# Kernel optimization log

Hardware: AMD Instinct MI355X
Metric: run time of the kernel (lower is better)

Reference implementation:

```python
import jax, jax.numpy as jnp
import numpy as np

B, S, D = 4, 2048, 1024
H, DK, DV = 16, 64, 64
LN_EPS = 1e-5


def setup_inputs() -> dict:
    key = jax.random.key(0)
    ks = jax.random.split(key, 6)
    x = jax.random.normal(ks[0], (B, S, D), dtype=jnp.float32)
    # causal mask: True = masked position (j > i), broadcast over batch
    causal = jnp.triu(jnp.ones((S, S), dtype=bool), k=1)
    attention_mask = jnp.broadcast_to(causal, (B, S, S))
    scale = 1.0 / np.sqrt(D)
    w_q = jax.random.normal(ks[1], (D, H * DK), dtype=jnp.float32) * scale
    w_k = jax.random.normal(ks[2], (D, H * DK), dtype=jnp.float32) * scale
    w_v = jax.random.normal(ks[3], (D, H * DV), dtype=jnp.float32) * scale
    w_fc = jax.random.normal(ks[4], (H * DV, D), dtype=jnp.float32) * (1.0 / np.sqrt(H * DV))
    ln_gamma = jnp.ones((D,), dtype=jnp.float32)
    ln_beta = jnp.zeros((D,), dtype=jnp.float32)
    return {"x": x, "attention_mask": attention_mask, "w_q": w_q, "w_k": w_k,
            "w_v": w_v, "w_fc": w_fc, "ln_gamma": ln_gamma, "ln_beta": ln_beta}


def _layernorm(y, gamma, beta):
    mu = jnp.mean(y, axis=-1, keepdims=True)
    var = jnp.mean(jnp.square(y - mu), axis=-1, keepdims=True)
    return (y - mu) * jax.lax.rsqrt(var + LN_EPS) * gamma + beta


def reference(x, attention_mask, w_q, w_k, w_v, w_fc, ln_gamma, ln_beta):
    b, s, _ = x.shape
    # projections -> [b, h, s, dk/dv]
    q = (x @ w_q).reshape(b, s, H, DK).transpose(0, 2, 1, 3)
    k = (x @ w_k).reshape(b, s, H, DK).transpose(0, 2, 1, 3)
    v = (x @ w_v).reshape(b, s, H, DV).transpose(0, 2, 1, 3)
    # scaled dot-product attention with mask (True -> -1e9)
    scores = jnp.einsum('bhqd,bhkd->bhqk', q, k) / np.sqrt(DK)
    scores = jnp.where(attention_mask[:, None, :, :], jnp.float32(-1e9), scores)
    attn = jax.nn.softmax(scores, axis=-1)
    context = jnp.einsum('bhqk,bhkd->bhqd', attn, v)
    context = context.transpose(0, 2, 1, 3).reshape(b, s, H * DV)
    output = context @ w_fc
    out = _layernorm(output + x, ln_gamma, ln_beta)
    return out, attn
```

## Files before the change

### kernel.cpp

```cpp
#include <hip/hip_runtime.h>
#include <stdint.h>

#define S_LEN 2048
#define NHEAD 16

typedef short short8 __attribute__((ext_vector_type(8)));
typedef float f32x4 __attribute__((ext_vector_type(4)));
typedef unsigned short u16;

typedef __attribute__((address_space(1))) uint32_t AS1u32;
typedef __attribute__((address_space(3))) uint32_t AS3u32;

#define MFMA16(a, b, c) __builtin_amdgcn_mfma_f32_16x16x32_bf16((a), (b), (c), 0, 0, 0)

__device__ __forceinline__ void gload16(const void* g, void* l) {
  __builtin_amdgcn_global_load_lds((AS1u32*)g, (AS3u32*)l, 16, 0, 0);
}

__device__ __forceinline__ u16 f2bf(float f) {
  union { float f; uint32_t u; } c; c.f = f;
  return (u16)((c.u + 0x7fffu + ((c.u >> 16) & 1u)) >> 16);
}

__global__ __launch_bounds__(256) void prep_kernel(
    const float* __restrict__ x, u16* __restrict__ xb,
    const float* __restrict__ w0, const float* __restrict__ w1,
    const float* __restrict__ w2, const float* __restrict__ w3,
    u16* __restrict__ qkvT, u16* __restrict__ fcT) {
  __shared__ float t[32][33];
  int bid = blockIdx.x;
  if (bid < 8192) {
    size_t i = ((size_t)bid * 256 + threadIdx.x) * 4;
    f32x4 v = *(const f32x4*)(x + i);
    union { u16 h[4]; uint2 d; } o;
    o.h[0] = f2bf(v[0]); o.h[1] = f2bf(v[1]); o.h[2] = f2bf(v[2]); o.h[3] = f2bf(v[3]);
    *(uint2*)(xb + i) = o.d;
    return;
  }
  int r = bid - 8192;
  int z = r >> 10; r &= 1023;
  int bx = r & 31, by = r >> 5;
  const float* w = (z == 0) ? w0 : (z == 1) ? w1 : (z == 2) ? w2 : w3;
  u16* o = (z == 3) ? fcT : qkvT + (size_t)z * 1048576;
  float scale = (z == 0) ? 0.125f : 1.0f;
  int n0 = bx * 32, k0 = by * 32;
  int tx = threadIdx.x & 31, ty = threadIdx.x >> 5;
#pragma unroll
  for (int i = 0; i < 4; ++i) {
    int k = ty * 4 + i;
    t[k][tx] = w[(size_t)(k0 + k) * 1024 + n0 + tx];
  }
  __syncthreads();
#pragma unroll
  for (int i = 0; i < 4; ++i) {
    int n = ty * 4 + i;
    o[(size_t)(n0 + n) * 1024 + k0 + tx] = f2bf(t[tx][n] * scale);
  }
}

__device__ __forceinline__ void gemm_stage(const char* Ab, const char* Bb, u16* As, u16* Bs,
                                           int m0, int n0, int kbyte, int tid) {
#pragma unroll
  for (int i = 0; i < 2; ++i) {
    int cid = i * 256 + tid;
    int row = cid >> 2, c = cid & 3;
    int off = kbyte + ((c ^ ((row >> 1) & 3)) << 4);
    gload16(Ab + (size_t)(m0 + row) * 2048 + off, (char*)As + i * 4096 + (tid & ~63) * 16);
    gload16(Bb + (size_t)(n0 + row) * 2048 + off, (char*)Bs + i * 4096 + (tid & ~63) * 16);
  }
}

__global__ __launch_bounds__(256) void gemm_bt_kernel(
    const u16* __restrict__ A, const u16* __restrict__ BT,
    void* __restrict__ out, void* __restrict__ outv, int mode) {
  __shared__ u16 sh[128 * 128];
  u16* As = sh;
  u16* Bs = sh + 4096;
  const int tid = threadIdx.x;
  const int lane = tid & 63, wv = tid >> 6;
  const int l15 = lane & 15, h16 = lane >> 4;
  const int wr = wv >> 1, wc = wv & 1;
  const int m0 = blockIdx.x * 128, n0 = blockIdx.y * 128;
  const char* Ab = (const char*)A;
  const char* Bb = (const char*)BT;

  f32x4 acc[4][4];
#pragma unroll
  for (int i = 0; i < 4; ++i)
#pragma unroll
    for (int j = 0; j < 4; ++j) acc[i][j] = (f32x4){0.f, 0.f, 0.f, 0.f};

  gemm_stage(Ab, Bb, As, Bs, m0, n0, 0, tid);
  for (int kt = 0; kt < 32; ++kt) {
    __syncthreads();
    short8 a[4], b[4];
#pragma unroll
    for (int mf = 0; mf < 4; ++mf) {
      int row = wr * 64 + mf * 16 + l15;
      a[mf] = *(const short8*)((const char*)As + row * 64 + ((h16 ^ ((row >> 1) & 3)) << 4));
    }
#pragma unroll
    for (int nf = 0; nf < 4; ++nf) {
      int row = wc * 64 + nf * 16 + l15;
      b[nf] = *(const short8*)((const char*)Bs + row * 64 + ((h16 ^ ((row >> 1) & 3)) << 4));
    }
#pragma unroll
    for (int mf = 0; mf < 4; ++mf)
#pragma unroll
      for (int nf = 0; nf < 4; ++nf)
        acc[mf][nf] = MFMA16(a[mf], b[nf], acc[mf][nf]);
    __syncthreads();
    if (kt + 1 < 32) gemm_stage(Ab, Bb, As, Bs, m0, n0, (kt + 1) * 64, tid);
  }

  if (mode == 0 && n0 < 2048) {
    u16* o = (u16*)out;
#pragma unroll
    for (int mf = 0; mf < 4; ++mf)
#pragma unroll
      for (int nf = 0; nf < 4; ++nf)
#pragma unroll
        for (int r = 0; r < 4; ++r) {
          int row = wr * 64 + mf * 16 + 4 * h16 + r;
          int col = wc * 64 + nf * 16 + l15;
          *(u16*)((char*)sh + row * 256 + (((col >> 3) ^ (row & 7)) << 4) + (col & 7) * 2) =
              f2bf(acc[mf][nf][r]);
        }
    __syncthreads();
    int row = tid >> 1, hf = tid & 1;
    int m = m0 + row;
    int bb = m >> 11, s = m & 2047;
    int n_base = n0 + hf * 64;
    int z = n_base >> 10, nn = n_base & 1023, hh = nn >> 6;
    u16* dst = o + (size_t)z * 8388608 + (((size_t)(bb * NHEAD + hh) * S_LEN + s) << 6);
#pragma unroll
    for (int i = 0; i < 8; ++i) {
      int ch = hf * 8 + i;
      short8 v = *(const short8*)((const char*)sh + row * 256 + ((ch ^ (row & 7)) << 4));
      *(short8*)(dst + i * 8) = v;
    }
  } else if (mode == 0) {
    u16* o = (u16*)outv;
#pragma unroll
    for (int mf = 0; mf < 4; ++mf)
#pragma unroll
      for (int nf = 0; nf < 4; ++nf)
#pragma unroll
        for (int r = 0; r < 4; ++r) {
          int row = wr * 64 + mf * 16 + 4 * h16 + r;
          int col = wc * 64 + nf * 16 + l15;
          *(u16*)((char*)sh + col * 256 + (((row >> 3) ^ (col & 7)) << 4) + (row & 7) * 2) =
              f2bf(acc[mf][nf][r]);
        }
    __syncthreads();
    int col = tid >> 1, half = tid & 1;
    int bb = m0 >> 11, s0 = (m0 & 2047) + half * 64;
    int nn = n0 - 2048 + col;
    int hh = nn >> 6, dv = nn & 63;
    u16* dst = o + ((size_t)(bb * NHEAD + hh) * 64 + dv) * S_LEN + s0;
    const char* base = (const char*)sh + col * 256;
#pragma unroll
    for (int i = 0; i < 8; ++i) {
      int ch = (half * 8 + i) ^ (col & 7);
      *(short8*)(dst + i * 8) = *(const short8*)(base + (ch << 4));
    }
  } else {
    float* o = (float*)out;
#pragma unroll
    for (int mf = 0; mf < 4; ++mf)
#pragma unroll
      for (int nf = 0; nf < 4; ++nf)
#pragma unroll
        for (int r = 0; r < 4; ++r) {
          int m = m0 + wr * 64 + mf * 16 + 4 * h16 + r;
          int n = n0 + wc * 64 + nf * 16 + l15;
          o[(size_t)m * 1024 + n] = acc[mf][nf][r];
        }
  }
}

__device__ __forceinline__ void stage_qk(const char* base, int row0, u16* dst, int tid) {
#pragma unroll
  for (int i = 0; i < 2; ++i) {
    int cid = i * 512 + tid;
    int row = cid >> 3, c = cid & 7;
    gload16(base + (size_t)(row0 + row) * 128 + ((c ^ (row & 7)) << 4),
            (char*)dst + i * 8192 + (tid & ~63) * 16);
  }
}
__device__ __forceinline__ void stage_v(const char* Vb, int kv0, u16* dst, int tid) {
#pragma unroll
  for (int i = 0; i < 2; ++i) {
    int cid = i * 512 + tid;
    int row = cid >> 4, c = cid & 15;
    gload16(Vb + (size_t)row * 4096 + (size_t)kv0 * 2 + ((c ^ (row & 7)) << 4),
            (char*)dst + i * 8192 + (tid & ~63) * 16);
  }
}

__device__ __forceinline__ void qk_tile(const char* Kc, const short8* qf,
                                        f32x4* sc, int l15, int h16) {
#pragma unroll
  for (int nf = 0; nf < 8; ++nf) sc[nf] = (f32x4){0.f, 0.f, 0.f, 0.f};
#pragma unroll
  for (int ks = 0; ks < 2; ++ks)
#pragma unroll
    for (int nf = 0; nf < 8; ++nf) {
      int row = nf * 16 + l15;
      short8 kb = *(const short8*)(Kc + row * 128 + (((ks * 4 + h16) ^ (row & 7)) << 4));
      sc[nf] = MFMA16(qf[ks], kb, sc[nf]);
    }
}

__device__ __forceinline__ void attn_one(
    const u16* __restrict__ Q, const u16* __restrict__ K, const u16* __restrict__ VT,
    float* __restrict__ attn, u16* __restrict__ ctx, int qt, int bh, int tid,
    u16 (*Ks)[128 * 64], u16* Vs, u16* Ps) {
  const int lane = tid & 63, wv = tid >> 6;
  const int l15 = lane & 15, h16 = lane >> 4;
  const int w16 = wv * 16;
  const int q0 = qt * 128;
  const char* Qb = (const char*)(Q + (size_t)bh * S_LEN * 64);
  const char* Kb = (const char*)(K + (size_t)bh * S_LEN * 64);
  const char* Vb = (const char*)(VT + (size_t)bh * 64 * S_LEN);
  float* attb = attn + (size_t)bh * S_LEN * S_LEN;

  stage_qk(Qb, q0, Ps, tid);
  stage_qk(Kb, q0, Ks[0], tid);
  __syncthreads();
  short8 qf[2];
  {
    int row = w16 + l15;
    qf[0] = *(const short8*)((const char*)Ps + row * 128 + ((h16 ^ (row & 7)) << 4));
    qf[1] = *(const short8*)((const char*)Ps + row * 128 + (((4 + h16) ^ (row & 7)) << 4));
  }
  __syncthreads();

  float lsum[4] = {0.f, 0.f, 0.f, 0.f};
  int cur = 0;
  for (int t = qt; t >= 0; --t) {
    if (t > 0) stage_qk(Kb, (t - 1) * 128, Ks[cur ^ 1], tid);
    f32x4 sc[8];
    qk_tile((const char*)Ks[cur], qf, sc, l15, h16);
    if (t == qt) {
#pragma unroll
      for (int nf = 0; nf < 8; ++nf)
#pragma unroll
        for (int r = 0; r < 4; ++r)
          if (nf * 16 + l15 > w16 + 4 * h16 + r) sc[nf][r] = -1e30f;
    }
#pragma unroll
    for (int nf = 0; nf < 8; ++nf)
#pragma unroll
      for (int r = 0; r < 4; ++r) lsum[r] += __expf(sc[nf][r]);
    __syncthreads();
    cur ^= 1;
  }
  cur ^= 1;
  f32x4 ri;
#pragma unroll
  for (int r = 0; r < 4; ++r) {
    float v = lsum[r];
    v += __shfl_xor(v, 1);
    v += __shfl_xor(v, 2);
    v += __shfl_xor(v, 4);
    v += __shfl_xor(v, 8);
    ri[r] = 1.0f / v;
  }

  f32x4 cacc[4];
#pragma unroll
  for (int nf = 0; nf < 4; ++nf) cacc[nf] = (f32x4){0.f, 0.f, 0.f, 0.f};

  for (int t = 0; t <= qt; ++t) {
    const int kv0 = t * 128;
    stage_v(Vb, kv0, Vs, tid);
    f32x4 sc[8];
    qk_tile((const char*)Ks[cur], qf, sc, l15, h16);
    if (t == qt) {
#pragma unroll
      for (int nf = 0; nf < 8; ++nf)
#pragma unroll
        for (int r = 0; r < 4; ++r)
          if (nf * 16 + l15 > w16 + 4 * h16 + r) sc[nf][r] = -1e30f;
    }
    {
      float* arow = attb + (size_t)(q0 + w16 + 4 * h16) * S_LEN + kv0 + l15;
#pragma unroll
      for (int nf = 0; nf < 8; ++nf)
#pragma unroll
        for (int r = 0; r < 4; ++r) {
          float p = __expf(sc[nf][r]) * ri[r];
          int rowL = w16 + 4 * h16 + r;
          int chunk = 2 * nf + (l15 >> 3);
          *(u16*)((char*)Ps + rowL * 256 + ((chunk ^ (rowL & 7)) << 4) + (l15 & 7) * 2) = f2bf(p);
          arow[(size_t)r * S_LEN + nf * 16] = p;
        }
    }
    __syncthreads();
    if (t < qt) stage_qk(Kb, kv0 + 128, Ks[cur ^ 1], tid);
#pragma unroll
    for (int ks = 0; ks < 4; ++ks) {
      int rowP = w16 + l15;
      short8 pa = *(const short8*)((const char*)Ps + rowP * 256 + (((ks * 4 + h16) ^ (rowP & 7)) << 4));
#pragma unroll
      for (int nf = 0; nf < 4; ++nf) {
        int rowV = nf * 16 + l15;
        short8 vbf = *(const short8*)((const char*)Vs + rowV * 256 + (((ks * 4 + h16) ^ (rowV & 7)) << 4));
        cacc[nf] = MFMA16(pa, vbf, cacc[nf]);
      }
    }
    __syncthreads();
    cur ^= 1;
  }

  for (int kvt = qt + 1; kvt < 16; ++kvt) {
    const int kv0 = kvt * 128;
    int row = tid >> 2, sub = tid & 3;
    float* arow = attb + (size_t)(q0 + row) * S_LEN + kv0;
    f32x4 z = {0.f, 0.f, 0.f, 0.f};
#pragma unroll
    for (int c8 = 0; c8 < 4; ++c8) {
      int chunk = sub + 4 * c8;
      *(f32x4*)(arow + chunk * 8) = z;
      *(f32x4*)(arow + chunk * 8 + 4) = z;
    }
  }

  {
    int b = bh >> 4, hh = bh & 15;
#pragma unroll
    for (int nf = 0; nf < 4; ++nf)
#pragma unroll
      for (int r = 0; r < 4; ++r) {
        int qrow = q0 + w16 + 4 * h16 + r;
        ctx[((size_t)b * S_LEN + qrow) * 1024 + hh * 64 + nf * 16 + l15] = f2bf(cacc[nf][r]);
      }
  }
}

__global__ __launch_bounds__(512) void attn2_kernel(
    const u16* __restrict__ Q, const u16* __restrict__ K, const u16* __restrict__ VT,
    float* __restrict__ attn, u16* __restrict__ ctx) {
  __shared__ u16 Ks[2][128 * 64];
  __shared__ u16 Vs[64 * 128];
  __shared__ u16 Ps[128 * 128];
  const int tid = threadIdx.x;
  const int w = blockIdx.x;
  const int bx = (w >> 3) & 7;
  const int bh = (w & 7) + ((w >> 6) << 3);
  attn_one(Q, K, VT, attn, ctx, 15 - bx, bh, tid, Ks, Vs, Ps);
  attn_one(Q, K, VT, attn, ctx, bx, bh, tid, Ks, Vs, Ps);
}

__global__ __launch_bounds__(256) void ln_kernel(float* __restrict__ io,
                                                 const float* __restrict__ x,
                                                 const float* __restrict__ gamma,
                                                 const float* __restrict__ beta) {
  int row = blockIdx.x, tid = threadIdx.x;
  size_t base = (size_t)row * 1024 + tid * 4;
  f32x4 p = *(const f32x4*)(io + base);
  f32x4 xv = *(const f32x4*)(x + base);
  f32x4 y;
  float s1 = 0.f, s2 = 0.f;
#pragma unroll
  for (int j = 0; j < 4; ++j) {
    y[j] = p[j] + xv[j];
    s1 += y[j];
    s2 += y[j] * y[j];
  }
#pragma unroll
  for (int off = 1; off <= 32; off <<= 1) {
    s1 += __shfl_xor(s1, off);
    s2 += __shfl_xor(s2, off);
  }
  __shared__ float r1[4], r2[4];
  int w = tid >> 6;
  if ((tid & 63) == 0) { r1[w] = s1; r2[w] = s2; }
  __syncthreads();
  float S1 = r1[0] + r1[1] + r1[2] + r1[3];
  float S2 = r2[0] + r2[1] + r2[2] + r2[3];
  float mu = S1 * (1.f / 1024.f);
  float var = S2 * (1.f / 1024.f) - mu * mu;
  float rs = rsqrtf(var + 1e-5f);
  f32x4 g = *(const f32x4*)(gamma + tid * 4);
  f32x4 bt = *(const f32x4*)(beta + tid * 4);
  f32x4 o;
#pragma unroll
  for (int j = 0; j < 4; ++j) o[j] = (y[j] - mu) * rs * g[j] + bt[j];
  *(f32x4*)(io + base) = o;
}

extern "C" void kernel_launch(void* const* d_in, const int* in_sizes, int n_in,
                              void* d_out, int out_size, void* d_ws, size_t ws_size,
                              hipStream_t stream) {
  (void)in_sizes; (void)n_in; (void)out_size; (void)ws_size;
  const float* x = (const float*)d_in[0];
  const float* wq = (const float*)d_in[2];
  const float* wk = (const float*)d_in[3];
  const float* wv = (const float*)d_in[4];
  const float* wfc = (const float*)d_in[5];
  const float* gamma = (const float*)d_in[6];
  const float* beta = (const float*)d_in[7];

  char* ws = (char*)d_ws;
  u16* xb = (u16*)ws;
  u16* wqkvT = (u16*)(ws + (16u << 20));
  u16* wfcT = (u16*)(ws + (22u << 20));
  u16* qkb = (u16*)(ws + (24u << 20));
  u16* qb = qkb;
  u16* kb = qkb + (size_t)8388608;
  u16* vT = (u16*)(ws + (56u << 20));
  u16* ctx = xb;

  float* outp = (float*)d_out;
  float* attnp = outp + (size_t)4 * 2048 * 1024;

  prep_kernel<<<12288, 256, 0, stream>>>(x, xb, wq, wk, wv, wfc, wqkvT, wfcT);
  gemm_bt_kernel<<<dim3(64, 24), 256, 0, stream>>>(xb, wqkvT, qkb, vT, 0);
  attn2_kernel<<<512, 512, 0, stream>>>(qb, kb, vT, attnp, ctx);
  gemm_bt_kernel<<<dim3(64, 8), 256, 0, stream>>>(ctx, wfcT, outp, nullptr, 1);
  ln_kernel<<<8192, 256, 0, stream>>>(outp, x, gamma, beta);
}
```

Measured before the change: 473.1 us.

## Fuse row-sum passes of paired query tiles to share K tile loads

The attention kernel handles two query tiles per block (a high and a low causal tile). It previously ran a separate softmax-denominator pass for each, and now runs a single K sweep that computes row sums for both tiles from the same K fragments held in LDS. This removes the duplicated K staging and LDS reads of the low tile's first pass. It also adds a launch_bounds occupancy hint, at the cost of more live registers for the second set of Q fragments and accumulators.

```diff
diff --git a/kernel.cpp b/kernel.cpp
--- a/kernel.cpp
+++ b/kernel.cpp
@@ -212,61 +212,14 @@
     }
 }
 
-__device__ __forceinline__ void attn_one(
-    const u16* __restrict__ Q, const u16* __restrict__ K, const u16* __restrict__ VT,
-    float* __restrict__ attn, u16* __restrict__ ctx, int qt, int bh, int tid,
-    u16 (*Ks)[128 * 64], u16* Vs, u16* Ps) {
+__device__ __forceinline__ void attn_emit(
+    const char* Kb, const char* Vb, float* attb, u16* __restrict__ ctx,
+    int qt, int bh, int tid, const short8* qf, f32x4 ri,
+    u16 (*Ks)[128 * 64], u16* Vs, u16* Ps, int cur) {
   const int lane = tid & 63, wv = tid >> 6;
   const int l15 = lane & 15, h16 = lane >> 4;
   const int w16 = wv * 16;
   const int q0 = qt * 128;
-  const char* Qb = (const char*)(Q + (size_t)bh * S_LEN * 64);
-  const char* Kb = (const char*)(K + (size_t)bh * S_LEN * 64);
-  const char* Vb = (const char*)(VT + (size_t)bh * 64 * S_LEN);
-  float* attb = attn + (size_t)bh * S_LEN * S_LEN;
-
-  stage_qk(Qb, q0, Ps, tid);
-  stage_qk(Kb, q0, Ks[0], tid);
-  __syncthreads();
-  short8 qf[2];
-  {
-    int row = w16 + l15;
-    qf[0] = *(const short8*)((const char*)Ps + row * 128 + ((h16 ^ (row & 7)) << 4));
-    qf[1] = *(const short8*)((const char*)Ps + row * 128 + (((4 + h16) ^ (row & 7)) << 4));
-  }
-  __syncthreads();
-
-  float lsum[4] = {0.f, 0.f, 0.f, 0.f};
-  int cur = 0;
-  for (int t = qt; t >= 0; --t) {
-    if (t > 0) stage_qk(Kb, (t - 1) * 128, Ks[cur ^ 1], tid);
-    f32x4 sc[8];
-    qk_tile((const char*)Ks[cur], qf, sc, l15, h16);
-    if (t == qt) {
-#pragma unroll
-      for (int nf = 0; nf < 8; ++nf)
-#pragma unroll
-        for (int r = 0; r < 4; ++r)
-          if (nf * 16 + l15 > w16 + 4 * h16 + r) sc[nf][r] = -1e30f;
-    }
-#pragma unroll
-    for (int nf = 0; nf < 8; ++nf)
-#pragma unroll
-      for (int r = 0; r < 4; ++r) lsum[r] += __expf(sc[nf][r]);
-    __syncthreads();
-    cur ^= 1;
-  }
-  cur ^= 1;
-  f32x4 ri;
-#pragma unroll
-  for (int r = 0; r < 4; ++r) {
-    float v = lsum[r];
-    v += __shfl_xor(v, 1);
-    v += __shfl_xor(v, 2);
-    v += __shfl_xor(v, 4);
-    v += __shfl_xor(v, 8);
-    ri[r] = 1.0f / v;
-  }
 
   f32x4 cacc[4];
 #pragma unroll
@@ -339,7 +292,103 @@
   }
 }
 
-__global__ __launch_bounds__(512) void attn2_kernel(
+__device__ __forceinline__ void attn_pair(
+    const u16* __restrict__ Q, const u16* __restrict__ K, const u16* __restrict__ VT,
+    float* __restrict__ attn, u16* __restrict__ ctx, int qtH, int qtL, int bh, int tid,
+    u16 (*Ks)[128 * 64], u16* Vs, u16* Ps) {
+  const int lane = tid & 63, wv = tid >> 6;
+  const int l15 = lane & 15, h16 = lane >> 4;
+  const int w16 = wv * 16;
+  const char* Qb = (const char*)(Q + (size_t)bh * S_LEN * 64);
+  const char* Kb = (const char*)(K + (size_t)bh * S_LEN * 64);
+  const char* Vb = (const char*)(VT + (size_t)bh * 64 * S_LEN);
+  float* attb = attn + (size_t)bh * S_LEN * S_LEN;
+
+  stage_qk(Qb, qtH * 128, Ps, tid);
+  stage_qk(Kb, qtH * 128, Ks[0], tid);
+  __syncthreads();
+  short8 qfh[2];
+  {
+    int row = w16 + l15;
+    qfh[0] = *(const short8*)((const char*)Ps + row * 128 + ((h16 ^ (row & 7)) << 4));
+    qfh[1] = *(const short8*)((const char*)Ps + row * 128 + (((4 + h16) ^ (row & 7)) << 4));
+  }
+  __syncthreads();
+  stage_qk(Qb, qtL * 128, Ps, tid);
+  __syncthreads();
+  short8 qfl[2];
+  {
+    int row = w16 + l15;
+    qfl[0] = *(const short8*)((const char*)Ps + row * 128 + ((h16 ^ (row & 7)) << 4));
+    qfl[1] = *(const short8*)((const char*)Ps + row * 128 + (((4 + h16) ^ (row & 7)) << 4));
+  }
+  __syncthreads();
+
+  float lsH[4] = {0.f, 0.f, 0.f, 0.f};
+  float lsL[4] = {0.f, 0.f, 0.f, 0.f};
+  int cur = 0;
+  for (int t = qtH; t >= 0; --t) {
+    if (t > 0) stage_qk(Kb, (t - 1) * 128, Ks[cur ^ 1], tid);
+    const char* Kc = (const char*)Ks[cur];
+    const bool doL = (t <= qtL);
+#pragma unroll
+    for (int nf = 0; nf < 8; ++nf) {
+      int row = nf * 16 + l15;
+      short8 k0 = *(const short8*)(Kc + row * 128 + ((h16 ^ (row & 7)) << 4));
+      short8 k1 = *(const short8*)(Kc + row * 128 + (((4 + h16) ^ (row & 7)) << 4));
+      f32x4 s = {0.f, 0.f, 0.f, 0.f};
+      s = MFMA16(qfh[0], k0, s);
+      s = MFMA16(qfh[1], k1, s);
+      if (t == qtH) {
+#pragma unroll
+        for (int r = 0; r < 4; ++r)
+          if (nf * 16 + l15 > w16 + 4 * h16 + r) s[r] = -1e30f;
+      }
+#pragma unroll
+      for (int r = 0; r < 4; ++r) lsH[r] += __expf(s[r]);
+      if (doL) {
+        f32x4 sl = {0.f, 0.f, 0.f, 0.f};
+        sl = MFMA16(qfl[0], k0, sl);
+        sl = MFMA16(qfl[1], k1, sl);
+        if (t == qtL) {
+#pragma unroll
+          for (int r = 0; r < 4; ++r)
+            if (nf * 16 + l15 > w16 + 4 * h16 + r) sl[r] = -1e30f;
+        }
+#pragma unroll
+        for (int r = 0; r < 4; ++r) lsL[r] += __expf(sl[r]);
+      }
+    }
+    __syncthreads();
+    cur ^= 1;
+  }
+  cur ^= 1;
+
+  f32x4 riH, riL;
+#pragma unroll
+  for (int r = 0; r < 4; ++r) {
+    float v = lsH[r];
+    v += __shfl_xor(v, 1);
+    v += __shfl_xor(v, 2);
+    v += __shfl_xor(v, 4);
+    v += __shfl_xor(v, 8);
+    riH[r] = 1.0f / v;
+    float u = lsL[r];
+    u += __shfl_xor(u, 1);
+    u += __shfl_xor(u, 2);
+    u += __shfl_xor(u, 4);
+    u += __shfl_xor(u, 8);
+    riL[r] = 1.0f / u;
+  }
+
+  attn_emit(Kb, Vb, attb, ctx, qtH, bh, tid, qfh, riH, Ks, Vs, Ps, cur);
+
+  stage_qk(Kb, 0, Ks[0], tid);
+  __syncthreads();
+  attn_emit(Kb, Vb, attb, ctx, qtL, bh, tid, qfl, riL, Ks, Vs, Ps, 0);
+}
+
+__global__ __launch_bounds__(512, 4) void attn2_kernel(
     const u16* __restrict__ Q, const u16* __restrict__ K, const u16* __restrict__ VT,
     float* __restrict__ attn, u16* __restrict__ ctx) {
   __shared__ u16 Ks[2][128 * 64];
@@ -349,8 +398,7 @@
   const int w = blockIdx.x;
   const int bx = (w >> 3) & 7;
   const int bh = (w & 7) + ((w >> 6) << 3);
-  attn_one(Q, K, VT, attn, ctx, 15 - bx, bh, tid, Ks, Vs, Ps);
-  attn_one(Q, K, VT, attn, ctx, bx, bh, tid, Ks, Vs, Ps);
+  attn_pair(Q, K, VT, attn, ctx, 15 - bx, bx, bh, tid, Ks, Vs, Ps);
 }
 
 __global__ __launch_bounds__(256) void ln_kernel(float* __restrict__ io,
```

Measured after the change: 603.7 us. 27.6% more time.
